# Optimization experiments

Hardware: AMD Instinct MI355X
Metric: run time of the kernel (lower is better)

Reference implementation:

```python
import jax, jax.numpy as jnp
import numpy as np

B, T, E, H, HD = 4, 1500, 1280, 20, 64
SCALING = HD ** -0.5


def setup_inputs() -> dict:
    key = jax.random.key(0)
    ks = jax.random.split(key, 8)
    s = 0.02
    return {
        "hidden_states": jax.random.normal(ks[0], (B, 1, T, E), jnp.float32),
        "attention_mask": jnp.zeros((B, 1, T, T), jnp.float32),
        "Wq": jax.random.normal(ks[1], (H, HD, E), jnp.float32) * s,
        "bq": jax.random.normal(ks[2], (H, HD), jnp.float32) * s,
        "Wk": jax.random.normal(ks[3], (H, HD, E), jnp.float32) * s,
        "Wv": jax.random.normal(ks[4], (H, HD, E), jnp.float32) * s,
        "bv": jax.random.normal(ks[5], (H, HD), jnp.float32) * s,
        "Wo": jax.random.normal(ks[6], (E, E), jnp.float32) * s,
        "bo": jax.random.normal(ks[7], (E,), jnp.float32) * s,
    }


def reference(hidden_states, attention_mask, Wq, bq, Wk, Wv, bv, Wo, bo):
    # hidden_states: [B, 1, T, E] (NHWC with H=1, as in the torch module)
    b, _, t, e = hidden_states.shape
    x = hidden_states[:, 0]  # [B, T, E]
    # Per-head 1x1 Conv2d projections == batched linear over stacked head weights.
    # Scaling is folded into q (the module bakes it into q_proj weights/bias).
    q = (jnp.einsum("bte,hde->bhtd", x, Wq) + bq[None, :, None, :]) * SCALING
    k = jnp.einsum("bse,hde->bhsd", x, Wk)
    v = jnp.einsum("bse,hde->bhsd", x, Wv) + bv[None, :, None, :]
    # attention_mask broadcasts over the head dim (module adds it per head as [B,1,T,S])
    scores = jnp.einsum("bhtd,bhsd->bhts", q, k) + attention_mask  # [B,H,T,S]
    attn = jax.nn.softmax(scores, axis=-1)
    out = jnp.einsum("bhts,bhsd->bhtd", attn, v)  # [B,H,T,HD]
    out = out.transpose(0, 2, 1, 3).reshape(b, t, e)  # concat heads on channel dim
    final = jnp.einsum("bte,fe->btf", out, Wo) + bo  # 1x1 Conv2d out_proj
    return final[:, None, :, :]  # [B,1,T,E]
```

## Files before the change

### kernel.cpp

```cpp
#include <hip/hip_runtime.h>

#define T_LEN 1500
#define TP    1536
#define EDIM  1280
#define NH    20
#define HD    64
#define KDIM  1280

#define OFF_X    ((size_t)0)
#define OFF_AO   ((size_t)0)
#define OFF_W    ((size_t)7700480)
#define OFF_WO   ((size_t)12615680)
#define OFF_Q    ((size_t)14254080)
#define OFF_K    ((size_t)22118400)
#define OFF_VT   ((size_t)29982720)

typedef float  f32x4  __attribute__((ext_vector_type(4)));
typedef float  f32x16 __attribute__((ext_vector_type(16)));
typedef short  s16x8  __attribute__((ext_vector_type(8)));
typedef __bf16 bf16x8 __attribute__((ext_vector_type(8)));
typedef unsigned short u16;
typedef unsigned int   u32;
typedef unsigned int u32x4 __attribute__((ext_vector_type(4)));

__device__ __forceinline__ f32x4 mfma_bf16(s16x8 a, s16x8 b, f32x4 c) {
  return __builtin_amdgcn_mfma_f32_16x16x32_bf16(
      __builtin_bit_cast(bf16x8, a), __builtin_bit_cast(bf16x8, b), c, 0, 0, 0);
}

__device__ __forceinline__ f32x16 mfma32(s16x8 a, s16x8 b, f32x16 c) {
  return __builtin_amdgcn_mfma_f32_32x32x16_bf16(
      __builtin_bit_cast(bf16x8, a), __builtin_bit_cast(bf16x8, b), c, 0, 0, 0);
}

__device__ __forceinline__ u16 f2bf(float f) {
  union { float f; unsigned int u; } a; a.f = f;
  return (u16)((a.u + 0x7fffu + ((a.u >> 16) & 1u)) >> 16);
}

__device__ __forceinline__ void gl_lds16(const u16* g, u16* l) {
  __builtin_amdgcn_global_load_lds(
      (const __attribute__((address_space(1))) unsigned int*)(const void*)g,
      (__attribute__((address_space(3))) unsigned int*)(void*)l, 16, 0, 0);
}


__global__ __launch_bounds__(256) void prep_kernel(
    const float* __restrict__ x, const float* __restrict__ wq,
    const float* __restrict__ wk, const float* __restrict__ wv,
    const float* __restrict__ wo, u16* __restrict__ ws) {
  const int S0 = 1925120;
  const int S1 = 1228800;
  const int S2 = 409600;
  const int P1 = 46080;
  const int TOT = S0 + S1 + S2 + 3 * P1;
  for (int v = blockIdx.x * 256 + threadIdx.x; v < TOT; v += gridDim.x * 256) {
    if (v < S0) {
      int i = v * 4;
      int m = i / EDIM;
      ushort4 o;
      if (m < 6000) {
        float4 f = *(const float4*)(x + i);
        o = make_ushort4(f2bf(f.x), f2bf(f.y), f2bf(f.z), f2bf(f.w));
      } else {
        o = make_ushort4(0, 0, 0, 0);
      }
      *(ushort4*)(ws + OFF_X + i) = o;
    } else if (v < S0 + S1) {
      int j = (v - S0) * 4;
      int n = j / EDIM, e = j - n * EDIM;
      const float* s = (n < 1280) ? wq + (size_t)n * EDIM + e
                     : (n < 2560) ? wk + (size_t)(n - 1280) * EDIM + e
                                  : wv + (size_t)(n - 2560) * EDIM + e;
      float4 f = *(const float4*)s;
      *(ushort4*)(ws + OFF_W + j) = make_ushort4(f2bf(f.x), f2bf(f.y), f2bf(f.z), f2bf(f.w));
    } else if (v < S0 + S1 + S2) {
      int j = (v - S0 - S1) * 4;
      float4 f = *(const float4*)(wo + j);
      *(ushort4*)(ws + OFF_WO + j) = make_ushort4(f2bf(f.x), f2bf(f.y), f2bf(f.z), f2bf(f.w));
    } else {
      int p = v - (S0 + S1 + S2);
      ushort4 z = make_ushort4(0, 0, 0, 0);
      if (p < P1) {
        int p4 = p * 4; int bh = p4 / 2304; int rem = p4 - bh * 2304;
        int tt = rem >> 6, d = rem & 63;
        *(ushort4*)(ws + OFF_Q + ((size_t)(bh * TP + 1500 + tt)) * HD + d) = z;
      } else if (p < 2 * P1) {
        int p4 = (p - P1) * 4; int bh = p4 / 2304; int rem = p4 - bh * 2304;
        int tt = rem >> 6, d = rem & 63;
        *(ushort4*)(ws + OFF_K + ((size_t)(bh * TP + 1500 + tt)) * HD + d) = z;
      } else {
        int p4 = (p - 2 * P1) * 4; int bh = p4 / 2304; int rem = p4 - bh * 2304;
        int d = rem / 36, ss = rem - d * 36;
        int t = 1500 + ss;
        int tphys = (t & ~63) | (((((t >> 3) & 7) ^ (d & 7))) << 3) | (t & 7);
        *(ushort4*)(ws + OFF_VT + ((size_t)(bh * HD + d)) * TP + tphys) = z;
      }
    }
  }
}

__device__ __forceinline__ void gemm_mainloop(
    const u16* __restrict__ A, const u16* __restrict__ B,
    int mt, int nt, u16* As, u16* Bs, f32x4 acc[4][4]) {
  const int tid = threadIdx.x;
  const int w = tid >> 6, lane = tid & 63, lg = lane >> 4, lr = lane & 15;
  const int wr = w >> 1, wc = w & 1;
  const int c0 = tid, c1 = tid + 256;
  const u16* a0 = A + (size_t)(mt * 128 + (c0 >> 2)) * KDIM + (c0 & 3) * 8;
  const u16* a1 = A + (size_t)(mt * 128 + (c1 >> 2)) * KDIM + (c1 & 3) * 8;
  const u16* b0 = B + (size_t)(nt * 128 + (c0 >> 2)) * KDIM + (c0 & 3) * 8;
  const u16* b1 = B + (size_t)(nt * 128 + (c1 >> 2)) * KDIM + (c1 & 3) * 8;
  u16* lA0 = As + c0 * 8; u16* lA1 = As + c1 * 8;
  u16* lB0 = Bs + c0 * 8; u16* lB1 = Bs + c1 * 8;
  for (int kt = 0; kt < KDIM / 32; ++kt) {
    gl_lds16(a0 + kt * 32, lA0);
    gl_lds16(a1 + kt * 32, lA1);
    gl_lds16(b0 + kt * 32, lB0);
    gl_lds16(b1 + kt * 32, lB1);
    __syncthreads();
    s16x8 af[4], bg[4];
    #pragma unroll
    for (int i = 0; i < 4; ++i) {
      af[i] = *(const s16x8*)(As + ((wr * 64 + i * 16 + lr) * 32 + lg * 8));
      bg[i] = *(const s16x8*)(Bs + ((wc * 64 + i * 16 + lr) * 32 + lg * 8));
    }
    #pragma unroll
    for (int i = 0; i < 4; ++i)
      #pragma unroll
      for (int j = 0; j < 4; ++j)
        acc[i][j] = mfma_bf16(af[i], bg[j], acc[i][j]);
    __syncthreads();
  }
}

__global__ __launch_bounds__(256) void gemm_qkv_kernel(
    const u16* __restrict__ X, const u16* __restrict__ W,
    const float* __restrict__ bq, const float* __restrict__ bv,
    u16* __restrict__ Qw, u16* __restrict__ Kw, u16* __restrict__ Vtw) {
  __shared__ __align__(16) u16 As[128 * 32];
  __shared__ __align__(16) u16 Bs[128 * 32];
  const int nt = blockIdx.x, mt = blockIdx.y;
  f32x4 acc[4][4] = {};
  gemm_mainloop(X, W, mt, nt, As, Bs, acc);
  const int tid = threadIdx.x;
  const int w = tid >> 6, lane = tid & 63, lg = lane >> 4, lr = lane & 15;
  const int wr = w >> 1, wc = w & 1;
  #pragma unroll
  for (int i = 0; i < 4; ++i) {
    #pragma unroll
    for (int r = 0; r < 4; ++r) {
      int mm = mt * 128 + wr * 64 + i * 16 + lg * 4 + r;
      if (mm >= 6000) continue;
      int bt = mm / 1500, tt = mm - bt * 1500;
      #pragma unroll
      for (int j = 0; j < 4; ++j) {
        int n = nt * 128 + wc * 64 + j * 16 + lr;
        float v = acc[i][j][r];
        if (n < 1280) {
          int hh = n >> 6, d = n & 63;
          Qw[((size_t)(bt * NH + hh) * TP + tt) * HD + d] = f2bf((v + bq[n]) * 0.125f);
        } else if (n < 2560) {
          int nn = n - 1280, hh = nn >> 6, d = nn & 63;
          int dp = ((((d >> 3) ^ (tt & 7))) << 3) | (d & 7);
          Kw[((size_t)(bt * NH + hh) * TP + tt) * HD + dp] = f2bf(v);
        } else {
          int nn = n - 2560, hh = nn >> 6, d = nn & 63;
          int tphys = (tt & ~63) | (((((tt >> 3) & 7) ^ (d & 7))) << 3) | (tt & 7);
          Vtw[((size_t)(bt * NH + hh) * HD + d) * TP + tphys] = f2bf(v + bv[nn]);
        }
      }
    }
  }
}

__global__ __launch_bounds__(256) void attn_kernel(
    const u16* __restrict__ Qw, const u16* __restrict__ Kw,
    const u16* __restrict__ Vtw, const float* __restrict__ mask,
    u16* __restrict__ AO) {
  __shared__ __align__(16) u16 Kb[2][64 * 64];
  __shared__ __align__(16) u16 Vb[2][64 * 64];
  const int bhid = blockIdx.y;
  const int bb = bhid / NH, hh = bhid % NH;
  const int tid = threadIdx.x;
  const int w = tid >> 6;
  const int lane = tid & 63;
  const int lq = lane & 31;
  const int hi = lane >> 5;
  const int q0 = blockIdx.x * 128 + w * 32;
  const int qrow = q0 + lq;
  const int qm = qrow < (T_LEN - 1) ? qrow : (T_LEN - 1);
  const u16* Qp = Qw + (size_t)bhid * TP * HD;
  const u16* Kp = Kw + (size_t)bhid * TP * HD;
  const u16* Vp = Vtw + (size_t)bhid * HD * TP;
  const float* mp = mask + (size_t)bb * T_LEN * T_LEN + (size_t)qm * T_LEN;

  s16x8 qf[4];
  #pragma unroll
  for (int c = 0; c < 4; ++c)
    qf[c] = *(const s16x8*)(Qp + (size_t)qrow * HD + c * 16 + hi * 8);

  f32x16 O0 = {}, O1 = {};
  float m = -3e38f, l = 0.f;

  {
    gl_lds16(Kp + tid * 8,                 Kb[0] + tid * 8);
    gl_lds16(Kp + 2048 + tid * 8,          Kb[0] + 2048 + tid * 8);
    int r = tid >> 3, g = tid & 7;
    gl_lds16(Vp + (size_t)r * TP + g * 8,          Vb[0] + tid * 8);
    gl_lds16(Vp + (size_t)(r + 32) * TP + g * 8,   Vb[0] + 2048 + tid * 8);
  }
  __syncthreads();

  int buf = 0;
  #pragma unroll 1
  for (int st = 0; st < 24; ++st) {
    const int s0 = st * 64;
    if (st < 23) {
      const int sn = s0 + 64;
      gl_lds16(Kp + (size_t)sn * HD + tid * 8,        Kb[buf ^ 1] + tid * 8);
      gl_lds16(Kp + (size_t)sn * HD + 2048 + tid * 8, Kb[buf ^ 1] + 2048 + tid * 8);
      int r = tid >> 3, g = tid & 7;
      gl_lds16(Vp + (size_t)r * TP + sn + g * 8,        Vb[buf ^ 1] + tid * 8);
      gl_lds16(Vp + (size_t)(r + 32) * TP + sn + g * 8, Vb[buf ^ 1] + 2048 + tid * 8);
    }
    f32x4 mk[2][4];
    #pragma unroll
    for (int sh = 0; sh < 2; ++sh)
      #pragma unroll
      for (int g = 0; g < 4; ++g) {
        int sb = s0 + sh * 32 + 8 * g + 4 * hi;
        if (sb > T_LEN - 4) sb = T_LEN - 4;
        mk[sh][g] = *(const f32x4*)(mp + sb);
      }
    const u16* kb = Kb[buf];
    f32x16 S0a = {}, S1a = {};
    #pragma unroll
    for (int c = 0; c < 4; ++c) {
      int gc = 2 * c + hi;
      int gs = (gc ^ (lq & 7)) << 3;
      s16x8 k0 = *(const s16x8*)(kb + lq * 64 + gs);
      s16x8 k1 = *(const s16x8*)(kb + (32 + lq) * 64 + gs);
      S0a = mfma32(k0, qf[c], S0a);
      S1a = mfma32(k1, qf[c], S1a);
    }
    float p[32];
    #pragma unroll
    for (int r = 0; r < 16; ++r) p[r]      = S0a[r] + mk[0][r >> 2][r & 3];
    #pragma unroll
    for (int r = 0; r < 16; ++r) p[16 + r] = S1a[r] + mk[1][r >> 2][r & 3];
    if (st == 23) {
      if (hi) { p[12] = p[13] = p[14] = p[15] = -3e38f; }
      #pragma unroll
      for (int r = 16; r < 32; ++r) p[r] = -3e38f;
    }
    float t1[16];
    #pragma unroll
    for (int r = 0; r < 16; ++r) t1[r] = fmaxf(p[r], p[r + 16]);
    #pragma unroll
    for (int r = 0; r < 8; ++r) t1[r] = fmaxf(t1[r], t1[r + 8]);
    #pragma unroll
    for (int r = 0; r < 4; ++r) t1[r] = fmaxf(t1[r], t1[r + 4]);
    float mx = fmaxf(fmaxf(t1[0], t1[1]), fmaxf(t1[2], t1[3]));
    mx = fmaxf(mx, __shfl_xor(mx, 32));
    float mn = fmaxf(m, mx);
    float sc = __expf(m - mn);
    #pragma unroll
    for (int r = 0; r < 32; ++r) p[r] = __expf(p[r] - mn);
    float s1[16];
    #pragma unroll
    for (int r = 0; r < 16; ++r) s1[r] = p[r] + p[r + 16];
    #pragma unroll
    for (int r = 0; r < 8; ++r) s1[r] += s1[r + 8];
    #pragma unroll
    for (int r = 0; r < 4; ++r) s1[r] += s1[r + 4];
    float rs = (s1[0] + s1[1]) + (s1[2] + s1[3]);
    rs += __shfl_xor(rs, 32);
    l = l * sc + rs;
    m = mn;
    O0 *= sc;
    O1 *= sc;
    const u16* vb = Vb[buf];
    #pragma unroll
    for (int sh = 0; sh < 2; ++sh) {
      u32 pk[8];
      #pragma unroll
      for (int j = 0; j < 8; ++j)
        asm("v_cvt_pk_bf16_f32 %0, %1, %2"
            : "=v"(pk[j]) : "v"(p[sh * 16 + 2 * j]), "v"(p[sh * 16 + 2 * j + 1]));
      asm("v_permlane32_swap_b32 %0, %1" : "+v"(pk[0]), "+v"(pk[2]));
      asm("v_permlane32_swap_b32 %0, %1" : "+v"(pk[1]), "+v"(pk[3]));
      asm("v_permlane32_swap_b32 %0, %1" : "+v"(pk[4]), "+v"(pk[6]));
      asm("v_permlane32_swap_b32 %0, %1" : "+v"(pk[5]), "+v"(pk[7]));
      u32x4 ta = {pk[0], pk[1], pk[2], pk[3]};
      u32x4 tb = {pk[4], pk[5], pk[6], pk[7]};
      s16x8 pfa = __builtin_bit_cast(s16x8, ta);
      s16x8 pfb = __builtin_bit_cast(s16x8, tb);
      int ga = sh * 4 + hi, gb = sh * 4 + 2 + hi;
      {
        int d = lq;
        s16x8 va = *(const s16x8*)(vb + d * 64 + ((ga ^ (d & 7)) << 3));
        s16x8 vc = *(const s16x8*)(vb + d * 64 + ((gb ^ (d & 7)) << 3));
        O0 = mfma32(va, pfa, O0);
        O0 = mfma32(vc, pfb, O0);
      }
      {
        int d = 32 + lq;
        s16x8 va = *(const s16x8*)(vb + d * 64 + ((ga ^ (d & 7)) << 3));
        s16x8 vc = *(const s16x8*)(vb + d * 64 + ((gb ^ (d & 7)) << 3));
        O1 = mfma32(va, pfa, O1);
        O1 = mfma32(vc, pfb, O1);
      }
    }
    __syncthreads();
    buf ^= 1;
  }

  if (qrow < T_LEN) {
    float inv = 1.f / l;
    size_t base = ((size_t)(bb * T_LEN + qrow)) * EDIM + hh * HD;
    #pragma unroll
    for (int g = 0; g < 4; ++g) {
      ushort4 o0, o1;
      o0.x = f2bf(O0[4 * g + 0] * inv); o0.y = f2bf(O0[4 * g + 1] * inv);
      o0.z = f2bf(O0[4 * g + 2] * inv); o0.w = f2bf(O0[4 * g + 3] * inv);
      o1.x = f2bf(O1[4 * g + 0] * inv); o1.y = f2bf(O1[4 * g + 1] * inv);
      o1.z = f2bf(O1[4 * g + 2] * inv); o1.w = f2bf(O1[4 * g + 3] * inv);
      *(ushort4*)(AO + base + 8 * g + 4 * hi)      = o0;
      *(ushort4*)(AO + base + 32 + 8 * g + 4 * hi) = o1;
    }
  }
}

__global__ __launch_bounds__(256) void gemm_out_kernel(
    const u16* __restrict__ AOb, const u16* __restrict__ Wob,
    const float* __restrict__ bo, float* __restrict__ out) {
  __shared__ __align__(16) u16 As[128 * 32];
  __shared__ __align__(16) u16 Bs[128 * 32];
  const int nt = blockIdx.x, mt = blockIdx.y;
  f32x4 acc[4][4] = {};
  gemm_mainloop(AOb, Wob, mt, nt, As, Bs, acc);
  const int tid = threadIdx.x;
  const int w = tid >> 6, lane = tid & 63, lg = lane >> 4, lr = lane & 15;
  const int wr = w >> 1, wc = w & 1;
  #pragma unroll
  for (int i = 0; i < 4; ++i) {
    #pragma unroll
    for (int r = 0; r < 4; ++r) {
      int mm = mt * 128 + wr * 64 + i * 16 + lg * 4 + r;
      if (mm >= 6000) continue;
      #pragma unroll
      for (int j = 0; j < 4; ++j) {
        int n = nt * 128 + wc * 64 + j * 16 + lr;
        out[(size_t)mm * EDIM + n] = acc[i][j][r] + bo[n];
      }
    }
  }
}

extern "C" void kernel_launch(void* const* d_in, const int* in_sizes, int n_in,
                              void* d_out, int out_size, void* d_ws, size_t ws_size,
                              hipStream_t stream) {
  const float* x    = (const float*)d_in[0];
  const float* mask = (const float*)d_in[1];
  const float* wq   = (const float*)d_in[2];
  const float* bq   = (const float*)d_in[3];
  const float* wk   = (const float*)d_in[4];
  const float* wv   = (const float*)d_in[5];
  const float* bv   = (const float*)d_in[6];
  const float* wo   = (const float*)d_in[7];
  const float* bo   = (const float*)d_in[8];
  float* out = (float*)d_out;
  u16* ws = (u16*)d_ws;

  prep_kernel<<<2048, 256, 0, stream>>>(x, wq, wk, wv, wo, ws);
  gemm_qkv_kernel<<<dim3(30, 47), 256, 0, stream>>>(
      ws + OFF_X, ws + OFF_W, bq, bv, ws + OFF_Q, ws + OFF_K, ws + OFF_VT);
  attn_kernel<<<dim3(12, 80), 256, 0, stream>>>(
      ws + OFF_Q, ws + OFF_K, ws + OFF_VT, mask, ws + OFF_AO);
  gemm_out_kernel<<<dim3(10, 47), 256, 0, stream>>>(
      ws + OFF_AO, ws + OFF_WO, bo, out);
}
```

Before: 288.6 us.

## Skip all-zero mask tiles via precomputed flags, use exp2 with lazy rescaling

The prep kernel now scans the attention mask and sets a flag for each 128x64 query/key tile that holds any nonzero value. The attention kernel loads and adds the mask only for flagged tiles, which avoids re-reading the fp32 mask once per head. Softmax moves to base 2: log2(e) is folded into the Q scale and exp2 replaces expf. Rescaling of the running max is skipped unless the new maximum exceeds the old by more than 8. The cost is a full extra pass over the mask plus a memset and atomics each call, and the flags live in scratch space inside the output buffer.

```diff
diff --git a/kernel.cpp b/kernel.cpp
--- a/kernel.cpp
+++ b/kernel.cpp
@@ -6,6 +6,8 @@
 #define NH    20
 #define HD    64
 #define KDIM  1280
+
+#define LOG2E 1.4426950408889634f
 
 #define OFF_X    ((size_t)0)
 #define OFF_AO   ((size_t)0)
@@ -38,6 +40,10 @@
   return (u16)((a.u + 0x7fffu + ((a.u >> 16) & 1u)) >> 16);
 }
 
+__device__ __forceinline__ float fexp2(float x) {
+  return __builtin_amdgcn_exp2f(x);
+}
+
 __device__ __forceinline__ void gl_lds16(const u16* g, u16* l) {
   __builtin_amdgcn_global_load_lds(
       (const __attribute__((address_space(1))) unsigned int*)(const void*)g,
@@ -48,12 +54,14 @@
 __global__ __launch_bounds__(256) void prep_kernel(
     const float* __restrict__ x, const float* __restrict__ wq,
     const float* __restrict__ wk, const float* __restrict__ wv,
-    const float* __restrict__ wo, u16* __restrict__ ws) {
+    const float* __restrict__ wo, const float* __restrict__ mask,
+    u16* __restrict__ ws, u32* __restrict__ nzflags) {
   const int S0 = 1925120;
   const int S1 = 1228800;
   const int S2 = 409600;
   const int P1 = 46080;
-  const int TOT = S0 + S1 + S2 + 3 * P1;
+  const int S3 = 2250000;
+  const int TOT = S0 + S1 + S2 + 3 * P1 + S3;
   for (int v = blockIdx.x * 256 + threadIdx.x; v < TOT; v += gridDim.x * 256) {
     if (v < S0) {
       int i = v * 4;
@@ -78,7 +86,7 @@
       int j = (v - S0 - S1) * 4;
       float4 f = *(const float4*)(wo + j);
       *(ushort4*)(ws + OFF_WO + j) = make_ushort4(f2bf(f.x), f2bf(f.y), f2bf(f.z), f2bf(f.w));
-    } else {
+    } else if (v < S0 + S1 + S2 + 3 * P1) {
       int p = v - (S0 + S1 + S2);
       ushort4 z = make_ushort4(0, 0, 0, 0);
       if (p < P1) {
@@ -96,6 +104,16 @@
         int tphys = (t & ~63) | (((((t >> 3) & 7) ^ (d & 7))) << 3) | (t & 7);
         *(ushort4*)(ws + OFF_VT + ((size_t)(bh * HD + d)) * TP + tphys) = z;
       }
+    } else {
+      int p = v - (S0 + S1 + S2 + 3 * P1);
+      int i4 = p * 4;
+      int bb = i4 / 2250000;
+      int rem = i4 - bb * 2250000;
+      int q = rem / 1500;
+      int s = rem - q * 1500;
+      float4 f = *(const float4*)(mask + (size_t)bb * 2250000 + rem);
+      if (f.x != 0.f || f.y != 0.f || f.z != 0.f || f.w != 0.f)
+        atomicOr(&nzflags[(bb * 12 + (q >> 7)) * 24 + (s >> 6)], 1u);
     }
   }
 }
@@ -159,7 +177,8 @@
         float v = acc[i][j][r];
         if (n < 1280) {
           int hh = n >> 6, d = n & 63;
-          Qw[((size_t)(bt * NH + hh) * TP + tt) * HD + d] = f2bf((v + bq[n]) * 0.125f);
+          Qw[((size_t)(bt * NH + hh) * TP + tt) * HD + d] =
+              f2bf((v + bq[n]) * (0.125f * LOG2E));
         } else if (n < 2560) {
           int nn = n - 1280, hh = nn >> 6, d = nn & 63;
           int dp = ((((d >> 3) ^ (tt & 7))) << 3) | (d & 7);
@@ -177,7 +196,7 @@
 __global__ __launch_bounds__(256) void attn_kernel(
     const u16* __restrict__ Qw, const u16* __restrict__ Kw,
     const u16* __restrict__ Vtw, const float* __restrict__ mask,
-    u16* __restrict__ AO) {
+    const u32* __restrict__ nzflags, u16* __restrict__ AO) {
   __shared__ __align__(16) u16 Kb[2][64 * 64];
   __shared__ __align__(16) u16 Vb[2][64 * 64];
   const int bhid = blockIdx.y;
@@ -194,6 +213,7 @@
   const u16* Kp = Kw + (size_t)bhid * TP * HD;
   const u16* Vp = Vtw + (size_t)bhid * HD * TP;
   const float* mp = mask + (size_t)bb * T_LEN * T_LEN + (size_t)qm * T_LEN;
+  const u32* nzp = nzflags + (bb * 12 + blockIdx.x) * 24;
 
   s16x8 qf[4];
   #pragma unroll
@@ -224,15 +244,7 @@
       gl_lds16(Vp + (size_t)r * TP + sn + g * 8,        Vb[buf ^ 1] + tid * 8);
       gl_lds16(Vp + (size_t)(r + 32) * TP + sn + g * 8, Vb[buf ^ 1] + 2048 + tid * 8);
     }
-    f32x4 mk[2][4];
-    #pragma unroll
-    for (int sh = 0; sh < 2; ++sh)
-      #pragma unroll
-      for (int g = 0; g < 4; ++g) {
-        int sb = s0 + sh * 32 + 8 * g + 4 * hi;
-        if (sb > T_LEN - 4) sb = T_LEN - 4;
-        mk[sh][g] = *(const f32x4*)(mp + sb);
-      }
+    const bool has_mask = nzp[st] != 0u;
     const u16* kb = Kb[buf];
     f32x16 S0a = {}, S1a = {};
     #pragma unroll
@@ -246,27 +258,44 @@
     }
     float p[32];
     #pragma unroll
-    for (int r = 0; r < 16; ++r) p[r]      = S0a[r] + mk[0][r >> 2][r & 3];
-    #pragma unroll
-    for (int r = 0; r < 16; ++r) p[16 + r] = S1a[r] + mk[1][r >> 2][r & 3];
+    for (int r = 0; r < 16; ++r) { p[r] = S0a[r]; p[16 + r] = S1a[r]; }
+    if (has_mask) {
+      f32x4 mk[2][4];
+      #pragma unroll
+      for (int sh = 0; sh < 2; ++sh)
+        #pragma unroll
+        for (int g = 0; g < 4; ++g) {
+          int sb = s0 + sh * 32 + 8 * g + 4 * hi;
+          if (sb > T_LEN - 4) sb = T_LEN - 4;
+          mk[sh][g] = *(const f32x4*)(mp + sb);
+        }
+      #pragma unroll
+      for (int r = 0; r < 16; ++r) {
+        p[r]      = fmaf(mk[0][r >> 2][r & 3], LOG2E, p[r]);
+        p[16 + r] = fmaf(mk[1][r >> 2][r & 3], LOG2E, p[16 + r]);
+      }
+    }
     if (st == 23) {
-      if (hi) { p[12] = p[13] = p[14] = p[15] = -3e38f; }
-      #pragma unroll
-      for (int r = 16; r < 32; ++r) p[r] = -3e38f;
+      if (hi) { p[12] = p[13] = p[14] = p[15] = -1e30f; }
+      #pragma unroll
+      for (int r = 16; r < 32; ++r) p[r] = -1e30f;
     }
     float t1[16];
     #pragma unroll
     for (int r = 0; r < 16; ++r) t1[r] = fmaxf(p[r], p[r + 16]);
     #pragma unroll
     for (int r = 0; r < 8; ++r) t1[r] = fmaxf(t1[r], t1[r + 8]);
-    #pragma unroll
-    for (int r = 0; r < 4; ++r) t1[r] = fmaxf(t1[r], t1[r + 4]);
-    float mx = fmaxf(fmaxf(t1[0], t1[1]), fmaxf(t1[2], t1[3]));
+    float mx = fmaxf(fmaxf(fmaxf(t1[0], t1[1]), fmaxf(t1[2], t1[3])),
+                     fmaxf(fmaxf(t1[4], t1[5]), fmaxf(t1[6], t1[7])));
     mx = fmaxf(mx, __shfl_xor(mx, 32));
-    float mn = fmaxf(m, mx);
-    float sc = __expf(m - mn);
-    #pragma unroll
-    for (int r = 0; r < 32; ++r) p[r] = __expf(p[r] - mn);
+    if (!__all(mx <= m + 8.f)) {
+      float mn = fmaxf(m, mx);
+      float sc = fexp2(m - mn);
+      O0 *= sc; O1 *= sc; l *= sc;
+      m = mn;
+    }
+    #pragma unroll
+    for (int r = 0; r < 32; ++r) p[r] = fexp2(p[r] - m);
     float s1[16];
     #pragma unroll
     for (int r = 0; r < 16; ++r) s1[r] = p[r] + p[r + 16];
@@ -276,10 +305,7 @@
     for (int r = 0; r < 4; ++r) s1[r] += s1[r + 4];
     float rs = (s1[0] + s1[1]) + (s1[2] + s1[3]);
     rs += __shfl_xor(rs, 32);
-    l = l * sc + rs;
-    m = mn;
-    O0 *= sc;
-    O1 *= sc;
+    l += rs;
     const u16* vb = Vb[buf];
     #pragma unroll
     for (int sh = 0; sh < 2; ++sh) {
@@ -372,12 +398,14 @@
   const float* bo   = (const float*)d_in[8];
   float* out = (float*)d_out;
   u16* ws = (u16*)d_ws;
-
-  prep_kernel<<<2048, 256, 0, stream>>>(x, wq, wk, wv, wo, ws);
+  u32* nzflags = (u32*)d_out;
+
+  hipMemsetAsync(nzflags, 0, 1152 * sizeof(u32), stream);
+  prep_kernel<<<2048, 256, 0, stream>>>(x, wq, wk, wv, wo, mask, ws, nzflags);
   gemm_qkv_kernel<<<dim3(30, 47), 256, 0, stream>>>(
       ws + OFF_X, ws + OFF_W, bq, bv, ws + OFF_Q, ws + OFF_K, ws + OFF_VT);
   attn_kernel<<<dim3(12, 80), 256, 0, stream>>>(
-      ws + OFF_Q, ws + OFF_K, ws + OFF_VT, mask, ws + OFF_AO);
+      ws + OFF_Q, ws + OFF_K, ws + OFF_VT, mask, nzflags, ws + OFF_AO);
   gemm_out_kernel<<<dim3(10, 47), 256, 0, stream>>>(
       ws + OFF_AO, ws + OFF_WO, bo, out);
 }
```

New measurement: 262.7 us. 9.0% less time.
